# Kernel tuning notes

Hardware: AMD Instinct MI355X
Metric: run time of the kernel (lower is better)

## Reference

```python
import jax, jax.numpy as jnp
import numpy as np

RES = 32  # voxel grid resolution per axis (cfg.MODEL.NEURAL_POINTS.VOXEL_RES)


def upsample_ac(x, s):
    """Bilinear upsample with align_corners=True. x: [B,C,h,w] -> [B,C,h*s,w*s]."""
    if s == 1:
        return x
    B, C, h, w = x.shape
    H, W = h * s, w * s
    ys = jnp.arange(H, dtype=x.dtype) * ((h - 1) / (H - 1))
    xs = jnp.arange(W, dtype=x.dtype) * ((w - 1) / (W - 1))
    y0 = jnp.floor(ys).astype(jnp.int32)
    x0 = jnp.floor(xs).astype(jnp.int32)
    y1 = jnp.minimum(y0 + 1, h - 1)
    x1 = jnp.minimum(x0 + 1, w - 1)
    wy = (ys - y0.astype(x.dtype))[:, None]  # [H,1]
    wx = (xs - x0.astype(x.dtype))[None, :]  # [1,W]
    top = x[:, :, y0, :]
    bot = x[:, :, y1, :]
    a = top[..., x0]; b = top[..., x1]; c = bot[..., x0]; d = bot[..., x1]
    return (a * (1 - wx) + b * wx) * (1 - wy) + (c * (1 - wx) + d * wx) * wy


def vox_closest(pos):
    """construct_vox_points_closest: per occupied voxel, index of point closest to
    the voxel's point centroid. pos: [N,3] -> [RES^3] int32 indices."""
    N = pos.shape[0]
    Vn = RES ** 3
    mn = pos.min(0)
    mx = pos.max(0)
    vsz = (mx - mn) / RES  # obtain_voxel_size_based_grid_res
    coord = jnp.clip(jnp.floor((pos - mn) / vsz).astype(jnp.int32), 0, RES - 1)
    vid = (coord[:, 0] * RES + coord[:, 1]) * RES + coord[:, 2]  # [N]
    cnt = jax.ops.segment_sum(jnp.ones((N,), pos.dtype), vid, Vn)
    cen = jax.ops.segment_sum(pos, vid, Vn) / jnp.maximum(cnt, 1.0)[:, None]
    d = jnp.sum((pos - cen[vid]) ** 2, axis=-1)  # [N] dist^2 to own-voxel centroid
    dmin = jax.ops.segment_min(d, vid, Vn)
    cand = jnp.where(d <= dmin[vid], jnp.arange(N, dtype=jnp.int32), N)
    midx = jax.ops.segment_min(cand, vid, Vn)
    return jnp.where(midx >= N, 0, midx)  # guard (rare) empty voxels


def reference(rgb, f1, f2, f3, points_pos, points_dir, W1, b1, W2, b2, points_mask):
    V, _, H, W = rgb.shape
    N = V * H * W
    C = 59
    # valid_index = where(points_mask == 1) (mask is all ones -> identity gather)
    valid = jnp.nonzero(points_mask[0] == 1, size=N, fill_value=0)[0]
    pos = points_pos[0, valid]          # [N,3]
    pdir = points_dir[0, valid]         # [N,3]
    # project_point_feats: upsample each pyramid level to full res, concat channels
    ups = [upsample_ac(rgb, 1), upsample_ac(f1, 2), upsample_ac(f2, 4), upsample_ac(f3, 8)]
    pif = jnp.concatenate(ups, axis=1)                       # [V,59,H,W]
    pif = jnp.transpose(pif, (0, 2, 3, 1)).reshape(N, C)     # [N,59]
    color = jax.lax.stop_gradient(jnp.transpose(rgb, (0, 2, 3, 1)).reshape(N, 3))
    pif = pif[valid]
    color = color[valid]
    emb = jnp.concatenate([pif, pdir], axis=-1)              # [N,62]
    midx = vox_closest(pos)                                  # [32768]
    sel_emb = emb[midx]
    sel_pos = pos[midx]
    sel_color = color[midx]
    sel_dir = pdir[midx]
    # point_mlp (premlp_init): 62 -> 256 -> 256
    h = jax.nn.relu(sel_emb @ W1 + b1)
    points_embedding = h @ W2 + b2
    return points_embedding, sel_pos, sel_color, sel_dir


def setup_inputs() -> dict:
    key = jax.random.key(0)
    ks = jax.random.split(key, 10)
    V, H, W = 8, 240, 320
    N = V * H * W
    return {
        "rgb": jax.random.uniform(ks[0], (V, 3, H, W), jnp.float32),
        "f1": jax.random.normal(ks[1], (V, 8, H // 2, W // 2), jnp.float32),
        "f2": jax.random.normal(ks[2], (V, 16, H // 4, W // 4), jnp.float32),
        "f3": jax.random.normal(ks[3], (V, 32, H // 8, W // 8), jnp.float32),
        "points_pos": jax.random.uniform(ks[4], (1, N, 3), jnp.float32),
        "points_dir": jax.random.normal(ks[5], (1, N, 3), jnp.float32),
        "W1": jax.random.normal(ks[6], (62, 256), jnp.float32) * 0.05,
        "b1": jnp.zeros((256,), jnp.float32),
        "W2": jax.random.normal(ks[7], (256, 256), jnp.float32) * 0.05,
        "b2": jnp.zeros((256,), jnp.float32),
        "points_mask": jnp.ones((1, N), jnp.int32),
    }
```

## Files before the change

kernel.cpp:

```cpp
#include <hip/hip_runtime.h>
#include <hip/hip_bf16.h>
#include <limits.h>
#include <stddef.h>

#define NPTS   614400
#define RESV   32
#define NVOX   (RESV*RESV*RESV)
#define IMG_H  240
#define IMG_W  320
#define IMG_HW (IMG_H*IMG_W)
#define INF    __builtin_inff()
#define CAP    64
#define SPILLCAP 4096

typedef __attribute__((ext_vector_type(8))) short short8;
typedef __attribute__((ext_vector_type(4))) short s16x4;
typedef __attribute__((ext_vector_type(4))) float f32x4;
typedef float f32x4u __attribute__((ext_vector_type(4), aligned(4)));

__device__ __forceinline__ float fadd_(float a, float b){
#pragma clang fp contract(off)
  return a + b;
}
__device__ __forceinline__ float fsub_(float a, float b){
#pragma clang fp contract(off)
  return a - b;
}
__device__ __forceinline__ float fmul_(float a, float b){
#pragma clang fp contract(off)
  return a * b;
}
__device__ __forceinline__ float fdiv_(float a, float b){
#pragma clang fp contract(off)
  return a / b;
}

__device__ __forceinline__ short f2bf(float x){
  __hip_bfloat16 h = __float2bfloat16(x);
  return *reinterpret_cast<short*>(&h);
}

__global__ void k_prep(int* __restrict__ cnt, int* __restrict__ spillcnt,
                       const float* __restrict__ W1, const float* __restrict__ W2,
                       short* __restrict__ W1t, short* __restrict__ W2t,
                       const float* __restrict__ pos,
                       f32x4* __restrict__ pmin, f32x4* __restrict__ pmax){
  int gid = blockIdx.x*blockDim.x + threadIdx.x;
  if (gid < NVOX) cnt[gid] = 0;
  if (gid == 0) *spillcnt = 0;
  if (gid < 256*64){
    int n = gid >> 6, k = gid & 63;
    W1t[gid] = (k < 62) ? f2bf(W1[k*256 + n]) : (short)0;
  } else if (gid < 256*64 + 256*256){
    int j = gid - 256*64;
    int n = j >> 8, k = j & 255;
    W2t[j] = f2bf(W2[k*256 + n]);
  }

  const f32x4* p4 = (const f32x4*)pos;
  float mn[3] = {  INF,  INF,  INF };
  float mx[3] = { -INF, -INF, -INF };
  int stride = gridDim.x*blockDim.x;
  for (int t = gid; t < NPTS/4; t += stride){
    f32x4 a = p4[3*t+0], b = p4[3*t+1], c = p4[3*t+2];
    mn[0] = fminf(mn[0], fminf(fminf(a.x, a.w), fminf(b.z, c.y)));
    mx[0] = fmaxf(mx[0], fmaxf(fmaxf(a.x, a.w), fmaxf(b.z, c.y)));
    mn[1] = fminf(mn[1], fminf(fminf(a.y, b.x), fminf(b.w, c.z)));
    mx[1] = fmaxf(mx[1], fmaxf(fmaxf(a.y, b.x), fmaxf(b.w, c.z)));
    mn[2] = fminf(mn[2], fminf(fminf(a.z, b.y), fminf(c.x, c.w)));
    mx[2] = fmaxf(mx[2], fmaxf(fmaxf(a.z, b.y), fmaxf(c.x, c.w)));
  }
  #pragma unroll
  for (int off = 32; off >= 1; off >>= 1){
    #pragma unroll
    for (int c = 0; c < 3; c++){
      mn[c] = fminf(mn[c], __shfl_down(mn[c], off, 64));
      mx[c] = fmaxf(mx[c], __shfl_down(mx[c], off, 64));
    }
  }
  __shared__ float smn[4][3], smx[4][3];
  int lane = threadIdx.x & 63, w = threadIdx.x >> 6;
  if (lane == 0){
    #pragma unroll
    for (int c = 0; c < 3; c++){ smn[w][c] = mn[c]; smx[w][c] = mx[c]; }
  }
  __syncthreads();
  if (threadIdx.x == 0){
    f32x4 a, b;
    a.x = fminf(fminf(smn[0][0], smn[1][0]), fminf(smn[2][0], smn[3][0]));
    a.y = fminf(fminf(smn[0][1], smn[1][1]), fminf(smn[2][1], smn[3][1]));
    a.z = fminf(fminf(smn[0][2], smn[1][2]), fminf(smn[2][2], smn[3][2]));
    a.w = 0.f;
    b.x = fmaxf(fmaxf(smx[0][0], smx[1][0]), fmaxf(smx[2][0], smx[3][0]));
    b.y = fmaxf(fmaxf(smx[0][1], smx[1][1]), fmaxf(smx[2][1], smx[3][1]));
    b.z = fmaxf(fmaxf(smx[0][2], smx[1][2]), fmaxf(smx[2][2], smx[3][2]));
    b.w = 0.f;
    pmin[blockIdx.x] = a;
    pmax[blockIdx.x] = b;
  }
}

__device__ __forceinline__ void reduce_minmax(const f32x4* __restrict__ pmin,
                                              const f32x4* __restrict__ pmax,
                                              float mn[3], float vsz[3]){
  int t = threadIdx.x;
  f32x4 a = pmin[t], b = pmin[t+256];
  f32x4 c = pmax[t], d = pmax[t+256];
  float lmn[3] = { fminf(a.x,b.x), fminf(a.y,b.y), fminf(a.z,b.z) };
  float lmx[3] = { fmaxf(c.x,d.x), fmaxf(c.y,d.y), fmaxf(c.z,d.z) };
  #pragma unroll
  for (int off = 32; off >= 1; off >>= 1){
    #pragma unroll
    for (int k = 0; k < 3; k++){
      lmn[k] = fminf(lmn[k], __shfl_xor(lmn[k], off, 64));
      lmx[k] = fmaxf(lmx[k], __shfl_xor(lmx[k], off, 64));
    }
  }
  __shared__ float smn[4][3], smx[4][3];
  int lane = t & 63, w = t >> 6;
  if (lane == 0){
    #pragma unroll
    for (int k = 0; k < 3; k++){ smn[w][k] = lmn[k]; smx[w][k] = lmx[k]; }
  }
  __syncthreads();
  #pragma unroll
  for (int k = 0; k < 3; k++){
    mn[k] = fminf(fminf(smn[0][k], smn[1][k]), fminf(smn[2][k], smn[3][k]));
    float mx = fmaxf(fmaxf(smx[0][k], smx[1][k]), fmaxf(smx[2][k], smx[3][k]));
    vsz[k] = fdiv_(fsub_(mx, mn[k]), 32.0f);
  }
}

__global__ void k_scatter(const float* __restrict__ pos,
                          const f32x4* __restrict__ pmin, const f32x4* __restrict__ pmax,
                          int* __restrict__ cnt, int* __restrict__ slots,
                          int* __restrict__ spillcnt, int2* __restrict__ spill){
  float mn[3], vsz[3];
  reduce_minmax(pmin, pmax, mn, vsz);

  int t = blockIdx.x*blockDim.x + threadIdx.x;
  const f32x4* p4 = (const f32x4*)pos;
  f32x4 a = p4[3*t+0], b = p4[3*t+1], c = p4[3*t+2];
  float X[4] = {a.x, a.w, b.z, c.y};
  float Y[4] = {a.y, b.x, b.w, c.z};
  float Z[4] = {a.z, b.y, c.x, c.w};
  #pragma unroll
  for (int j = 0; j < 4; j++){
    int i = 4*t + j;
    float P[3] = {X[j], Y[j], Z[j]};
    int v = 0;
    #pragma unroll
    for (int k = 0; k < 3; k++){
      float tt = fdiv_(fsub_(P[k], mn[k]), vsz[k]);
      int cc = (int)floorf(tt);
      cc = min(max(cc, 0), RESV-1);
      v = v*RESV + cc;
    }
    int p = atomicAdd(&cnt[v], 1);
    if (p < CAP){
      slots[v*CAP + p] = i;
    } else {
      int sp = atomicAdd(spillcnt, 1);
      if (sp < SPILLCAP){ int2 e; e.x = v; e.y = i; spill[sp] = e; }
    }
  }
}

__launch_bounds__(256)
__global__ void k_voxfull(const int* __restrict__ cnt, const int* __restrict__ slots,
                          const int* __restrict__ spillcnt, const int2* __restrict__ spill,
                          const float* __restrict__ pos,
                          const float* __restrict__ pdir, const float* __restrict__ rgb,
                          const float* __restrict__ f1, const float* __restrict__ f2,
                          const float* __restrict__ f3,
                          float* __restrict__ selpos, float* __restrict__ selcol,
                          float* __restrict__ seldir, short* __restrict__ emb){
  int lane = threadIdx.x & 63;
  int v = blockIdx.x*4 + (threadIdx.x >> 6);
  int n = cnt[v];
  int m = 0;
  unsigned long long ball = 0;
  float px = 0.f, py = 0.f, pz = 0.f;

  if (n > CAP){
    if (lane == 0){
      int sc = min(*spillcnt, SPILLCAP);
      float sx = 0.f, sy = 0.f, sz = 0.f; int last = -1;
      for (int i = 0; i < n; i++){
        int best = INT_MAX;
        for (int j = 0; j < CAP; j++){
          int id = slots[v*CAP + j];
          if (id > last && id < best) best = id;
        }
        for (int j = 0; j < sc; j++){
          int2 e = spill[j];
          if (e.x == v && e.y > last && e.y < best) best = e.y;
        }
        sx = fadd_(sx, pos[3*best+0]);
        sy = fadd_(sy, pos[3*best+1]);
        sz = fadd_(sz, pos[3*best+2]);
        last = best;
      }
      float cf = (float)n;
      float cx = fdiv_(sx, cf), cy = fdiv_(sy, cf), cz = fdiv_(sz, cf);
      float dmin = INF; int mm = 0;
      for (int j = 0; j < CAP + sc; j++){
        int id; int ok = 1;
        if (j < CAP) id = slots[v*CAP + j];
        else { int2 e = spill[j-CAP]; ok = (e.x == v); id = e.y; }
        if (!ok) continue;
        float dx = fsub_(pos[3*id+0], cx);
        float dy = fsub_(pos[3*id+1], cy);
        float dz = fsub_(pos[3*id+2], cz);
        float d  = fadd_(fadd_(fmul_(dx,dx), fmul_(dy,dy)), fmul_(dz,dz));
        if (d < dmin || (d == dmin && id < mm)){ dmin = d; mm = id; }
      }
      m = mm;
    }
    m = __shfl(m, 0, 64);
  } else {
    int key = INT_MAX;
    float gx = 0.f, gy = 0.f, gz = 0.f;
    if (lane < n){
      key = slots[v*CAP + lane];
      if (key < NPTS-1){
        f32x4u q = *(const f32x4u*)&pos[3*key];
        gx = q.x; gy = q.y; gz = q.z;
      } else {
        gx = pos[3*key+0]; gy = pos[3*key+1]; gz = pos[3*key+2];
      }
    }
    int src = lane;
    #pragma unroll
    for (int k = 2; k <= 64; k <<= 1){
      #pragma unroll
      for (int j = k >> 1; j >= 1; j >>= 1){
        int ok = __shfl_xor(key, j, 64);
        int os = __shfl_xor(src, j, 64);
        bool up    = ((lane & k) == 0);
        bool lower = ((lane & j) == 0);
        bool sw = (lower == up) ? (ok < key) : (ok > key);
        if (sw){ key = ok; src = os; }
      }
    }
    px = __shfl(gx, src, 64);
    py = __shfl(gy, src, 64);
    pz = __shfl(gz, src, 64);

    float sx = 0.f, sy = 0.f, sz = 0.f;
    for (int i = 0; i < n; i++){
      sx = fadd_(sx, __shfl(px, i, 64));
      sy = fadd_(sy, __shfl(py, i, 64));
      sz = fadd_(sz, __shfl(pz, i, 64));
    }
    float cf = fmaxf((float)n, 1.0f);
    float cx = fdiv_(sx, cf), cy = fdiv_(sy, cf), cz = fdiv_(sz, cf);

    float bd = INF; int bi = 0;
    if (lane < n){
      float dx = fsub_(px, cx), dy = fsub_(py, cy), dz = fsub_(pz, cz);
      bd = fadd_(fadd_(fmul_(dx,dx), fmul_(dy,dy)), fmul_(dz,dz));
      bi = key;
    }
    #pragma unroll
    for (int off = 32; off >= 1; off >>= 1){
      float od = __shfl_xor(bd, off, 64);
      int   oi = __shfl_xor(bi, off, 64);
      if (od < bd || (od == bd && oi < bi)){ bd = od; bi = oi; }
    }
    m = bi;
    ball = __ballot(lane < n && key == m);
  }

  float wx_ = 0.f, wy_ = 0.f, wz_ = 0.f;
  if (ball){
    int wl = (int)(__ffsll((long long)ball) - 1);
    wx_ = __shfl(px, wl, 64);
    wy_ = __shfl(py, wl, 64);
    wz_ = __shfl(pz, wl, 64);
  }

  int img = m / IMG_HW;
  int rem = m - img*IMG_HW;
  int y = rem / IMG_W;
  int x = rem - y*IMG_W;
  int ch = lane;
  float val;
  if (ch < 3){
    val = rgb[((img*3 + ch)*IMG_H + y)*IMG_W + x];
    selcol[3*v+ch] = val;
    float sp = ball ? ((ch == 0) ? wx_ : (ch == 1) ? wy_ : wz_) : pos[3*m+ch];
    selpos[3*v+ch] = sp;
  } else if (ch < 59){
    int lvl = (ch >= 27) ? 2 : ((ch >= 11) ? 1 : 0);
    const float* f = (lvl == 0) ? f1 : ((lvl == 1) ? f2 : f3);
    int c   = ch - ((lvl == 0) ? 3 : ((lvl == 1) ? 11 : 27));
    int C   = 8 << lvl;
    int h   = 120 >> lvl, w = 160 >> lvl;
    float ry = (lvl == 0) ? (119.0f/239.0f) : ((lvl == 1) ? (59.0f/239.0f) : (29.0f/239.0f));
    float rx = (lvl == 0) ? (159.0f/319.0f) : ((lvl == 1) ? (79.0f/319.0f) : (39.0f/319.0f));
    float ys = (float)y * ry;
    float xs = (float)x * rx;
    int y0 = (int)floorf(ys);
    int x0 = (int)floorf(xs);
    int y1 = min(y0+1, h-1);
    int x1 = min(x0+1, w-1);
    float wy = ys - (float)y0;
    float wx = xs - (float)x0;
    const float* plane = f + ((size_t)img*C + c)*(size_t)(h*w);
    float aa = plane[y0*w + x0];
    float bb = plane[y0*w + x1];
    float cc = plane[y1*w + x0];
    float dd = plane[y1*w + x1];
    val = (aa*(1.f-wx) + bb*wx)*(1.f-wy) + (cc*(1.f-wx) + dd*wx)*wy;
  } else if (ch < 62){
    val = pdir[3*m + (ch-59)];
    seldir[3*v+(ch-59)] = val;
  } else {
    val = 0.f;
  }
  emb[(size_t)v*64 + ch] = f2bf(val);
}

#define MLP_BLOCKS 512
#define MLP_TILES  (NVOX/16/MLP_BLOCKS)
__launch_bounds__(256, 2)
__global__ void k_mlp(const short* __restrict__ emb, const short* __restrict__ W1t,
                      const float* __restrict__ b1f, const short* __restrict__ W2t,
                      const float* __restrict__ b2f, float* __restrict__ out){
  __shared__ short Hs[16][264];
  int t    = threadIdx.x;
  int lane = t & 63;
  int wv   = t >> 6;
  int m    = lane & 15;
  int q    = lane >> 4;

  short8 w1f[4][2], w2f[4][8];
  float  b1r[4][4], b2r[4];
  #pragma unroll
  for (int nt = 0; nt < 4; nt++){
    int n = wv*64 + nt*16 + m;
    #pragma unroll
    for (int kq = 0; kq < 2; kq++)
      w1f[nt][kq] = *(const short8*)&W1t[(size_t)n*64 + kq*32 + q*8];
    #pragma unroll
    for (int kq = 0; kq < 8; kq++)
      w2f[nt][kq] = *(const short8*)&W2t[(size_t)n*256 + kq*32 + q*8];
    #pragma unroll
    for (int i = 0; i < 4; i++)
      b1r[nt][i] = b1f[wv*64 + nt*16 + q*4 + i];
    b2r[nt] = b2f[n];
  }

  for (int tt = 0; tt < MLP_TILES; tt++){
    int row0 = (blockIdx.x*MLP_TILES + tt)*16;

    short8 ef0 = *(const short8*)&emb[(size_t)(row0 + m)*64 + q*8];
    short8 ef1 = *(const short8*)&emb[(size_t)(row0 + m)*64 + 32 + q*8];

    #pragma unroll
    for (int nt = 0; nt < 4; nt++){
      f32x4 c = {0.f, 0.f, 0.f, 0.f};
      c = __builtin_amdgcn_mfma_f32_16x16x32_bf16(w1f[nt][0], ef0, c, 0, 0, 0);
      c = __builtin_amdgcn_mfma_f32_16x16x32_bf16(w1f[nt][1], ef1, c, 0, 0, 0);
      s16x4 hv;
      #pragma unroll
      for (int i = 0; i < 4; i++)
        hv[i] = f2bf(fmaxf(c[i] + b1r[nt][i], 0.f));
      *(s16x4*)&Hs[m][wv*64 + nt*16 + q*4] = hv;
    }
    __syncthreads();

    f32x4 acc[4] = {{0,0,0,0},{0,0,0,0},{0,0,0,0},{0,0,0,0}};
    #pragma unroll
    for (int kq = 0; kq < 8; kq++){
      short8 af = *(const short8*)&Hs[m][kq*32 + q*8];
      #pragma unroll
      for (int nt = 0; nt < 4; nt++)
        acc[nt] = __builtin_amdgcn_mfma_f32_16x16x32_bf16(af, w2f[nt][kq], acc[nt], 0, 0, 0);
    }
    __syncthreads();

    #pragma unroll
    for (int nt = 0; nt < 4; nt++){
      int n = wv*64 + nt*16 + m;
      #pragma unroll
      for (int i = 0; i < 4; i++)
        out[(size_t)(row0 + q*4 + i)*256 + n] = acc[nt][i] + b2r[nt];
    }
  }
}

extern "C" void kernel_launch(void* const* d_in, const int* in_sizes, int n_in,
                              void* d_out, int out_size, void* d_ws, size_t ws_size,
                              hipStream_t stream){
  const float* rgb  = (const float*)d_in[0];
  const float* f1   = (const float*)d_in[1];
  const float* f2   = (const float*)d_in[2];
  const float* f3   = (const float*)d_in[3];
  const float* pos  = (const float*)d_in[4];
  const float* pdir = (const float*)d_in[5];
  const float* W1   = (const float*)d_in[6];
  const float* b1   = (const float*)d_in[7];
  const float* W2   = (const float*)d_in[8];
  const float* b2   = (const float*)d_in[9];

  float* out      = (float*)d_out;
  float* out_emb  = out;
  float* out_pos  = out + (size_t)NVOX*256;
  float* out_col  = out_pos + (size_t)NVOX*3;
  float* out_dir  = out_col + (size_t)NVOX*3;

  char* w = (char*)d_ws;
  int*   spillcnt = (int*)w;       w += 64;
  f32x4* pmin     = (f32x4*)w;     w += (size_t)512*16;
  f32x4* pmax     = (f32x4*)w;     w += (size_t)512*16;
  int*   cnt      = (int*)w;       w += (size_t)NVOX*4;
  short* W1t      = (short*)w;     w += (size_t)256*64*2;
  short* W2t      = (short*)w;     w += (size_t)256*256*2;
  short* emb      = (short*)w;     w += (size_t)NVOX*64*2;
  int2*  spill    = (int2*)w;      w += (size_t)SPILLCAP*8;
  int*   slots    = (int*)w;       w += (size_t)NVOX*CAP*4;

  k_prep    <<<512,    256, 0, stream>>>(cnt, spillcnt, W1, W2, W1t, W2t, pos, pmin, pmax);
  k_scatter <<<NPTS/1024, 256, 0, stream>>>(pos, pmin, pmax, cnt, slots, spillcnt, spill);
  k_voxfull <<<NVOX/4, 256, 0, stream>>>(cnt, slots, spillcnt, spill,
                                         pos, pdir, rgb, f1, f2, f3,
                                         out_pos, out_col, out_dir, emb);
  k_mlp     <<<MLP_BLOCKS, 256, 0, stream>>>(emb, W1t, b1, W2t, b2, out_emb);
}
```

Baseline: 198.9 us.

## Transpose pyramid feature maps to channel-last for coalesced bilinear gathers

In the prep kernel, the f1/f2/f3 feature maps are transposed from CHW planes to HWC layout in workspace, when the workspace is large enough to hold them. k_voxfull then reads the four bilinear corners from the transposed copy, so adjacent lanes handling adjacent channels hit contiguous addresses instead of strided planes. The cost is one extra full pass over the feature maps (about 9.8 MB read and written) inside k_prep, plus extra workspace.

```diff
diff --git a/kernel.cpp b/kernel.cpp
--- a/kernel.cpp
+++ b/kernel.cpp
@@ -44,8 +44,13 @@
                        const float* __restrict__ W1, const float* __restrict__ W2,
                        short* __restrict__ W1t, short* __restrict__ W2t,
                        const float* __restrict__ pos,
-                       f32x4* __restrict__ pmin, f32x4* __restrict__ pmax){
+                       f32x4* __restrict__ pmin, f32x4* __restrict__ pmax,
+                       const float* __restrict__ f1, const float* __restrict__ f2,
+                       const float* __restrict__ f3,
+                       float* __restrict__ f1t, float* __restrict__ f2t,
+                       float* __restrict__ f3t, int tposed){
   int gid = blockIdx.x*blockDim.x + threadIdx.x;
+  int stride = gridDim.x*blockDim.x;
   if (gid < NVOX) cnt[gid] = 0;
   if (gid == 0) *spillcnt = 0;
   if (gid < 256*64){
@@ -57,10 +62,44 @@
     W2t[j] = f2bf(W2[k*256 + n]);
   }
 
+  if (tposed){
+    for (int p = gid; p < 8*19200; p += stride){
+      int img = p / 19200, pix = p - img*19200;
+      const float* s = f1 + (size_t)img*8*19200 + pix;
+      float r[8];
+      #pragma unroll
+      for (int c = 0; c < 8; c++) r[c] = s[(size_t)c*19200];
+      float* d = f1t + (size_t)p*8;
+      *(f32x4*)&d[0] = (f32x4){r[0],r[1],r[2],r[3]};
+      *(f32x4*)&d[4] = (f32x4){r[4],r[5],r[6],r[7]};
+    }
+    for (int p = gid; p < 8*4800; p += stride){
+      int img = p / 4800, pix = p - img*4800;
+      const float* s = f2 + (size_t)img*16*4800 + pix;
+      float* d = f2t + (size_t)p*16;
+      #pragma unroll
+      for (int cq = 0; cq < 4; cq++){
+        f32x4 v = { s[(size_t)(4*cq+0)*4800], s[(size_t)(4*cq+1)*4800],
+                    s[(size_t)(4*cq+2)*4800], s[(size_t)(4*cq+3)*4800] };
+        *(f32x4*)&d[4*cq] = v;
+      }
+    }
+    for (int p = gid; p < 8*1200; p += stride){
+      int img = p / 1200, pix = p - img*1200;
+      const float* s = f3 + (size_t)img*32*1200 + pix;
+      float* d = f3t + (size_t)p*32;
+      #pragma unroll
+      for (int cq = 0; cq < 8; cq++){
+        f32x4 v = { s[(size_t)(4*cq+0)*1200], s[(size_t)(4*cq+1)*1200],
+                    s[(size_t)(4*cq+2)*1200], s[(size_t)(4*cq+3)*1200] };
+        *(f32x4*)&d[4*cq] = v;
+      }
+    }
+  }
+
   const f32x4* p4 = (const f32x4*)pos;
   float mn[3] = {  INF,  INF,  INF };
   float mx[3] = { -INF, -INF, -INF };
-  int stride = gridDim.x*blockDim.x;
   for (int t = gid; t < NPTS/4; t += stride){
     f32x4 a = p4[3*t+0], b = p4[3*t+1], c = p4[3*t+2];
     mn[0] = fminf(mn[0], fminf(fminf(a.x, a.w), fminf(b.z, c.y)));
@@ -173,6 +212,8 @@
                           const float* __restrict__ pdir, const float* __restrict__ rgb,
                           const float* __restrict__ f1, const float* __restrict__ f2,
                           const float* __restrict__ f3,
+                          const float* __restrict__ f1t, const float* __restrict__ f2t,
+                          const float* __restrict__ f3t, int tposed,
                           float* __restrict__ selpos, float* __restrict__ selcol,
                           float* __restrict__ seldir, short* __restrict__ emb){
   int lane = threadIdx.x & 63;
@@ -293,7 +334,6 @@
     selpos[3*v+ch] = sp;
   } else if (ch < 59){
     int lvl = (ch >= 27) ? 2 : ((ch >= 11) ? 1 : 0);
-    const float* f = (lvl == 0) ? f1 : ((lvl == 1) ? f2 : f3);
     int c   = ch - ((lvl == 0) ? 3 : ((lvl == 1) ? 11 : 27));
     int C   = 8 << lvl;
     int h   = 120 >> lvl, w = 160 >> lvl;
@@ -307,11 +347,22 @@
     int x1 = min(x0+1, w-1);
     float wy = ys - (float)y0;
     float wx = xs - (float)x0;
-    const float* plane = f + ((size_t)img*C + c)*(size_t)(h*w);
-    float aa = plane[y0*w + x0];
-    float bb = plane[y0*w + x1];
-    float cc = plane[y1*w + x0];
-    float dd = plane[y1*w + x1];
+    float aa, bb, cc, dd;
+    if (tposed){
+      const float* ft = (lvl == 0) ? f1t : ((lvl == 1) ? f2t : f3t);
+      const float* base = ft + (size_t)(img*h*w)*C + c;
+      aa = base[(y0*w + x0)*C];
+      bb = base[(y0*w + x1)*C];
+      cc = base[(y1*w + x0)*C];
+      dd = base[(y1*w + x1)*C];
+    } else {
+      const float* f = (lvl == 0) ? f1 : ((lvl == 1) ? f2 : f3);
+      const float* plane = f + ((size_t)img*C + c)*(size_t)(h*w);
+      aa = plane[y0*w + x0];
+      bb = plane[y0*w + x1];
+      cc = plane[y1*w + x0];
+      dd = plane[y1*w + x1];
+    }
     val = (aa*(1.f-wx) + bb*wx)*(1.f-wy) + (cc*(1.f-wx) + dd*wx)*wy;
   } else if (ch < 62){
     val = pdir[3*m + (ch-59)];
@@ -421,11 +472,18 @@
   short* emb      = (short*)w;     w += (size_t)NVOX*64*2;
   int2*  spill    = (int2*)w;      w += (size_t)SPILLCAP*8;
   int*   slots    = (int*)w;       w += (size_t)NVOX*CAP*4;
-
-  k_prep    <<<512,    256, 0, stream>>>(cnt, spillcnt, W1, W2, W1t, W2t, pos, pmin, pmax);
+  float* f1t      = (float*)w;     w += (size_t)8*19200*8*4;
+  float* f2t      = (float*)w;     w += (size_t)8*4800*16*4;
+  float* f3t      = (float*)w;     w += (size_t)8*1200*32*4;
+
+  int tposed = ((size_t)(w - (char*)d_ws) <= ws_size) ? 1 : 0;
+
+  k_prep    <<<512,    256, 0, stream>>>(cnt, spillcnt, W1, W2, W1t, W2t, pos, pmin, pmax,
+                                         f1, f2, f3, f1t, f2t, f3t, tposed);
   k_scatter <<<NPTS/1024, 256, 0, stream>>>(pos, pmin, pmax, cnt, slots, spillcnt, spill);
   k_voxfull <<<NVOX/4, 256, 0, stream>>>(cnt, slots, spillcnt, spill,
                                          pos, pdir, rgb, f1, f2, f3,
+                                         f1t, f2t, f3t, tposed,
                                          out_pos, out_col, out_dir, emb);
   k_mlp     <<<MLP_BLOCKS, 256, 0, stream>>>(emb, W1t, b1, W2t, b2, out_emb);
 }
```

New measurement: 202.6 us. No clear change (+1.8%).
